# Performance work log

Measured on AMD Instinct MI355X. Metric: run time of the kernel, lower is better.

## Reference

```python
import jax, jax.numpy as jnp
import numpy as np

B, Q, V, H, U = 4, 256, 2048, 512, 128

def setup_inputs() -> dict:
    key = jax.random.key(0)
    ks = jax.random.split(key, 5)
    return {
        "queries": jax.random.normal(ks[0], (B, Q, H), dtype=jnp.float32),
        "values": jax.random.normal(ks[1], (B, V, H), dtype=jnp.float32),
        "w1": jax.random.normal(ks[2], (H, U), dtype=jnp.float32) / np.sqrt(H),
        "w2": jax.random.normal(ks[3], (H, U), dtype=jnp.float32) / np.sqrt(H),
        "v": jax.random.normal(ks[4], (U,), dtype=jnp.float32) / np.sqrt(U),
    }

def reference(queries, values, w1, w2, v):
    # Project queries and values first (cheap GEMMs), then broadcast-add.
    pq = jnp.einsum("bqh,hu->bqu", queries, w1)          # [B,Q,U]
    pv = jnp.einsum("bvh,hu->bvu", values, w2)           # [B,V,U]
    # added_qv: [B,Q,V,U] -- the large intermediate the original materializes
    scores = jnp.einsum("bqvu,u->bqv", jnp.tanh(pq[:, :, None, :] + pv[:, None, :, :]), v)
    attn = jax.nn.softmax(scores, axis=-1)               # softmax over V (last axis, as tf.nn.softmax)
    return jnp.einsum("bqv,bvh->bqh", attn, values)      # [B,Q,H]
```

## Files before the change

### kernel.cpp

```cpp
#include <hip/hip_runtime.h>

#define BB 4
#define QQ 256
#define VV 2048
#define HH 512
#define UU 128

#define C2E   2.8853900817779268f
#define LOG2E 1.4426950408889634f

__device__ __forceinline__ void fma4(float4& a, float s, const float4& w) {
    a.x = fmaf(s, w.x, a.x);
    a.y = fmaf(s, w.y, a.y);
    a.z = fmaf(s, w.z, a.z);
    a.w = fmaf(s, w.w, a.w);
}
__device__ __forceinline__ float2 rcp2(float2 x) {
    return make_float2(__builtin_amdgcn_rcpf(x.x), __builtin_amdgcn_rcpf(x.y));
}
__device__ __forceinline__ float2 mul2(float2 a, float2 b) { return make_float2(a.x*b.x, a.y*b.y); }
__device__ __forceinline__ float2 muls(float2 a, float s)  { return make_float2(a.x*s, a.y*s); }
__device__ __forceinline__ float2 fma2(float2 a, float2 b, float2 c) {
    return make_float2(fmaf(a.x, b.x, c.x), fmaf(a.y, b.y, c.y));
}
__device__ __forceinline__ float2 fmas(float2 a, float s, float2 c) {
    return make_float2(fmaf(a.x, s, c.x), fmaf(a.y, s, c.y));
}

__global__ __launch_bounds__(256) void proj_kernel(const float* __restrict__ queries,
                                                   const float* __restrict__ values,
                                                   const float* __restrict__ w1,
                                                   const float* __restrict__ w2,
                                                   float* __restrict__ pqI,
                                                   float* __restrict__ pvI,
                                                   float* __restrict__ denom) {
    __shared__ float smem[32 * 36 + 32 * 128];
    float (*As)[36] = (float(*)[36])smem;
    float* Ws = smem + 32 * 36;
    float (*Ls)[36] = (float(*)[36])smem;

    const int bid = blockIdx.x;
    const int tid = threadIdx.x;
    if (bid == 0) *(float4*)&denom[tid * 4] = make_float4(0.f, 0.f, 0.f, 0.f);

    const bool isv = (bid < 256);
    const float* A; const float* W; int b, r0, ROWS; float* Ob;
    if (isv) {
        b = bid >> 6; r0 = (bid & 63) * 32;
        A = values + ((size_t)(b * VV + r0)) * HH;  W = w2;
        Ob = pvI + (size_t)b * UU * VV;  ROWS = VV;
    } else {
        const int q = bid - 256;
        b = q >> 3; r0 = (q & 7) * 32;
        A = queries + ((size_t)(b * QQ + r0)) * HH; W = w1;
        Ob = pqI + (size_t)b * UU * QQ;  ROWS = QQ;
    }

    const int tx = tid & 31;
    const int ty = tid >> 5;
    float4 acc[4];
#pragma unroll
    for (int j = 0; j < 4; j++) acc[j] = make_float4(0.f, 0.f, 0.f, 0.f);

    for (int k0 = 0; k0 < HH; k0 += 32) {
        {
            const int r = tid >> 3, kk4 = (tid & 7) * 4;
            const float4 a = *(const float4*)&A[(size_t)r * HH + k0 + kk4];
            As[kk4 + 0][r] = a.x; As[kk4 + 1][r] = a.y;
            As[kk4 + 2][r] = a.z; As[kk4 + 3][r] = a.w;
        }
#pragma unroll
        for (int t = 0; t < 4; t++) {
            const int f = tid + t * 256;
            const int kk = f >> 5, u4 = (f & 31) * 4;
            *(float4*)&Ws[kk * 128 + u4] = *(const float4*)&W[(size_t)(k0 + kk) * UU + u4];
        }
        __syncthreads();
#pragma unroll
        for (int kk = 0; kk < 32; kk++) {
            const float4 a = *(const float4*)&As[kk][ty * 4];
            const float4 w = *(const float4*)&Ws[kk * 128 + tx * 4];
            fma4(acc[0], a.x, w);
            fma4(acc[1], a.y, w);
            fma4(acc[2], a.z, w);
            fma4(acc[3], a.w, w);
        }
        __syncthreads();
    }
#pragma unroll
    for (int j = 0; j < 4; j++) {
        const float aa[4] = {acc[j].x, acc[j].y, acc[j].z, acc[j].w};
#pragma unroll
        for (int i = 0; i < 4; i++)
            Ls[tx * 4 + i][ty * 4 + j] = __builtin_amdgcn_exp2f(aa[i] * C2E);
    }
    __syncthreads();
#pragma unroll
    for (int t = 0; t < 4; t++) {
        const int idx = tid + t * 256;
        const int g = idx >> 5, r = idx & 31;
        float4 o;
        o.x = Ls[4 * g + 0][r]; o.y = Ls[4 * g + 1][r];
        o.z = Ls[4 * g + 2][r]; o.w = Ls[4 * g + 3][r];
        *(float4*)&Ob[((size_t)g * ROWS + r0 + r) * 4] = o;
    }
}

__global__ __launch_bounds__(1024, 8) void fused_kernel(const float* __restrict__ pqI,
                                                        const float* __restrict__ pvI,
                                                        const float* __restrict__ vvec,
                                                        const float* __restrict__ values,
                                                        float* __restrict__ slab,
                                                        float* __restrict__ denom) {
    __shared__ float att[512][20];
    __shared__ float scratch[24 * 512];
    __shared__ float wred[8][16];
    const int tid = threadIdx.x;
    const int bid = blockIdx.x;
    const int vs = bid & 3, qb = (bid >> 2) & 15, b = bid >> 6;
    const int qbase = qb * 16, vbase = vs * 512;

    const int vloc = tid & 511;
    const int uh = tid >> 9;
    const int v = vbase + vloc;

    float vsum = 0.0f;
#pragma unroll
    for (int u4 = 0; u4 < UU; u4 += 4) {
        const float4 t = *(const float4*)&vvec[u4];
        vsum += t.x + t.y + t.z + t.w;
    }

    const float* pv4 = pvI + (size_t)b * UU * VV + (size_t)v * 4;
    const float* pq4 = pqI + (size_t)b * UU * QQ + (size_t)qbase * 4;

    float2 acc[8];
#pragma unroll
    for (int p = 0; p < 8; p++) acc[p] = make_float2(0.f, 0.f);

    const int G0 = uh * 16;
    float4 ev = *(const float4*)&pv4[(size_t)G0 * VV * 4];

    for (int g = 0; g < 16; g++) {
        const int G = G0 + g;
        const float* eqp = &pq4[(size_t)G * QQ * 4];
        float4 evn;
        if (g < 15) evn = *(const float4*)&pv4[(size_t)(G + 1) * VV * 4];
        const float4 wq = *(const float4*)&vvec[G * 4];
        const float w0 = 2.f * wq.x, w1 = 2.f * wq.y;
        const float w2 = 2.f * wq.z, w3 = 2.f * wq.w;
#pragma unroll
        for (int p = 0; p < 8; p++) {
            const float4 e0 = *(const float4*)&eqp[(2 * p) * 4];
            const float4 e1 = *(const float4*)&eqp[(2 * p + 1) * 4];
            const float2 a1 = make_float2(fmaf(e0.x, ev.x, 1.f), fmaf(e1.x, ev.x, 1.f));
            const float2 b1 = make_float2(fmaf(e0.y, ev.y, 1.f), fmaf(e1.y, ev.y, 1.f));
            const float2 c1 = make_float2(fmaf(e0.z, ev.z, 1.f), fmaf(e1.z, ev.z, 1.f));
            const float2 d1 = make_float2(fmaf(e0.w, ev.w, 1.f), fmaf(e1.w, ev.w, 1.f));
            const float2 pab = mul2(a1, b1), pcd = mul2(c1, d1);
            const float2 nab = fmas(a1, w1, muls(b1, w0));
            const float2 ncd = fmas(c1, w3, muls(d1, w2));
            const float2 num = fma2(nab, pcd, mul2(ncd, pab));
            const float2 den = mul2(pab, pcd);
            acc[p] = fma2(num, rcp2(den), acc[p]);
        }
        ev = evn;
    }

    float* cb = scratch;
    if (uh == 1) {
#pragma unroll
        for (int p = 0; p < 8; p++) {
            cb[(2 * p + 0) * 512 + vloc] = acc[p].x;
            cb[(2 * p + 1) * 512 + vloc] = acc[p].y;
        }
    }
    __syncthreads();
    if (uh == 0) {
#pragma unroll
        for (int p = 0; p < 8; p++) {
            const float hx = cb[(2 * p + 0) * 512 + vloc];
            const float hy = cb[(2 * p + 1) * 512 + vloc];
            float2 e;
            e.x = __builtin_amdgcn_exp2f((vsum - (acc[p].x + hx)) * LOG2E);
            e.y = __builtin_amdgcn_exp2f((vsum - (acc[p].y + hy)) * LOG2E);
            *(float2*)&att[vloc][2 * p] = e;
            acc[p] = e;
        }
#pragma unroll
        for (int off = 1; off < 64; off <<= 1) {
#pragma unroll
            for (int p = 0; p < 8; p++) {
                acc[p].x += __shfl_xor(acc[p].x, off, 64);
                acc[p].y += __shfl_xor(acc[p].y, off, 64);
            }
        }
        if ((tid & 63) == 0) {
            const int w = tid >> 6;
#pragma unroll
            for (int p = 0; p < 8; p++) {
                wred[w][2 * p + 0] = acc[p].x;
                wred[w][2 * p + 1] = acc[p].y;
            }
        }
    }
    __syncthreads();
    if (tid < 16) {
        float s = 0.f;
#pragma unroll
        for (int w = 0; w < 8; w++) s += wred[w][tid];
        atomicAdd(&denom[b * QQ + qbase + tid], s);
    }

    const int hg = tid & 127, sel = tid >> 7;
    const int qh = sel & 1, vh = sel >> 1;
    const int h0 = hg * 4;
    const float* vp = values + ((size_t)(b * VV + vbase + vh * 128)) * HH + h0;

    float4 oacc[8];
#pragma unroll
    for (int j = 0; j < 8; j++) oacc[j] = make_float4(0.f, 0.f, 0.f, 0.f);

#pragma unroll 2
    for (int vv = 0; vv < 128; vv++) {
        const float4 w = *(const float4*)&vp[(size_t)vv * HH];
        const float4 a0 = *(const float4*)&att[vh * 128 + vv][qh * 8 + 0];
        const float4 a1 = *(const float4*)&att[vh * 128 + vv][qh * 8 + 4];
        fma4(oacc[0], a0.x, w); fma4(oacc[1], a0.y, w);
        fma4(oacc[2], a0.z, w); fma4(oacc[3], a0.w, w);
        fma4(oacc[4], a1.x, w); fma4(oacc[5], a1.y, w);
        fma4(oacc[6], a1.z, w); fma4(oacc[7], a1.w, w);
    }

    float (*scr)[512] = (float(*)[512])scratch;
    for (int r = 0; r < 2; r++) {
        __syncthreads();
        if (qh == r && vh > 0) {
#pragma unroll
            for (int j = 0; j < 8; j++)
                *(float4*)&scr[(vh - 1) * 8 + j][h0] = oacc[j];
        }
        __syncthreads();
        if (qh == r && vh == 0) {
            float* sp = slab + (size_t)vs * (BB * QQ * HH);
#pragma unroll
            for (int j = 0; j < 8; j++) {
                const float4 p0 = *(const float4*)&scr[0 * 8 + j][h0];
                const float4 p1 = *(const float4*)&scr[1 * 8 + j][h0];
                const float4 p2 = *(const float4*)&scr[2 * 8 + j][h0];
                float4 o;
                o.x = oacc[j].x + p0.x + p1.x + p2.x;
                o.y = oacc[j].y + p0.y + p1.y + p2.y;
                o.z = oacc[j].z + p0.z + p1.z + p2.z;
                o.w = oacc[j].w + p0.w + p1.w + p2.w;
                *(float4*)&sp[((size_t)(b * QQ + qbase + r * 8 + j)) * HH + h0] = o;
            }
        }
    }
}

__global__ __launch_bounds__(256) void reduce_kernel(const float* __restrict__ slab,
                                                     const float* __restrict__ denom,
                                                     float* __restrict__ out) {
    const int i = blockIdx.x * 256 + threadIdx.x;
    const float r = __builtin_amdgcn_rcpf(denom[i >> 7]);
    const float4* s4 = (const float4*)slab;
    float4 s = s4[i];
#pragma unroll
    for (int k = 1; k < 4; k++) {
        const float4 p = s4[(size_t)k * (BB * QQ * HH / 4) + i];
        s.x += p.x; s.y += p.y; s.z += p.z; s.w += p.w;
    }
    s.x *= r; s.y *= r; s.z *= r; s.w *= r;
    ((float4*)out)[i] = s;
}

extern "C" void kernel_launch(void* const* d_in, const int* in_sizes, int n_in,
                              void* d_out, int out_size, void* d_ws, size_t ws_size,
                              hipStream_t stream) {
    const float* queries = (const float*)d_in[0];
    const float* values  = (const float*)d_in[1];
    const float* w1      = (const float*)d_in[2];
    const float* w2      = (const float*)d_in[3];
    const float* vvec    = (const float*)d_in[4];
    float* out = (float*)d_out;

    float* ws    = (float*)d_ws;
    float* pqI   = ws;
    float* pvI   = pqI + BB * UU * QQ;
    float* denom = pvI + (size_t)BB * UU * VV;
    float* slab  = denom + BB * QQ;

    proj_kernel<<<256 + 32, 256, 0, stream>>>(queries, values, w1, w2, pqI, pvI, denom);
    fused_kernel<<<BB * (QQ / 16) * (VV / 512), 1024, 0, stream>>>(pqI, pvI, vvec, values, slab, denom);
    reduce_kernel<<<(BB * QQ * HH) / 4 / 256, 256, 0, stream>>>(slab, denom, out);
}
```

Before: 173.8 us.

## Double-buffer proj kernel tiles with direct global-to-LDS weight loads

```diff
diff --git a/kernel.cpp b/kernel.cpp
--- a/kernel.cpp
+++ b/kernel.cpp
@@ -25,6 +25,12 @@
 }
 __device__ __forceinline__ float2 fmas(float2 a, float s, float2 c) {
     return make_float2(fmaf(a.x, s, c.x), fmaf(a.y, s, c.y));
+}
+
+typedef __attribute__((address_space(1))) const unsigned int g_u32;
+typedef __attribute__((address_space(3))) unsigned int l_u32;
+__device__ __forceinline__ void gl2lds16(const float* g, float* l) {
+    __builtin_amdgcn_global_load_lds((g_u32*)g, (l_u32*)l, 16, 0, 0);
 }
 
 __global__ __launch_bounds__(256) void proj_kernel(const float* __restrict__ queries,
@@ -34,9 +40,11 @@
                                                    float* __restrict__ pqI,
                                                    float* __restrict__ pvI,
                                                    float* __restrict__ denom) {
-    __shared__ float smem[32 * 36 + 32 * 128];
-    float (*As)[36] = (float(*)[36])smem;
-    float* Ws = smem + 32 * 36;
+    __shared__ float smem[2 * 1152 + 2 * 4096];
+    float* As0 = smem;
+    float* As1 = smem + 1152;
+    float* Ws0 = smem + 2304;
+    float* Ws1 = smem + 2304 + 4096;
     float (*Ls)[36] = (float(*)[36])smem;
 
     const int bid = blockIdx.x;
@@ -58,35 +66,59 @@
 
     const int tx = tid & 31;
     const int ty = tid >> 5;
+    const int lane = tid & 63, wv = tid >> 6;
+    const int r = tid >> 3, kk4 = (tid & 7) * 4;
+
     float4 acc[4];
 #pragma unroll
     for (int j = 0; j < 4; j++) acc[j] = make_float4(0.f, 0.f, 0.f, 0.f);
 
-    for (int k0 = 0; k0 < HH; k0 += 32) {
-        {
-            const int r = tid >> 3, kk4 = (tid & 7) * 4;
-            const float4 a = *(const float4*)&A[(size_t)r * HH + k0 + kk4];
-            As[kk4 + 0][r] = a.x; As[kk4 + 1][r] = a.y;
-            As[kk4 + 2][r] = a.z; As[kk4 + 3][r] = a.w;
-        }
-#pragma unroll
-        for (int t = 0; t < 4; t++) {
-            const int f = tid + t * 256;
-            const int kk = f >> 5, u4 = (f & 31) * 4;
-            *(float4*)&Ws[kk * 128 + u4] = *(const float4*)&W[(size_t)(k0 + kk) * UU + u4];
-        }
-        __syncthreads();
+    {
+#pragma unroll
+        for (int m = 0; m < 4; m++) {
+            const int c = wv * 4 + m;
+            gl2lds16(W + (size_t)c * 256 + lane * 4, Ws0 + c * 256);
+        }
+        const float4 a = *(const float4*)&A[(size_t)r * HH + kk4];
+        As0[(kk4 + 0) * 36 + r] = a.x; As0[(kk4 + 1) * 36 + r] = a.y;
+        As0[(kk4 + 2) * 36 + r] = a.z; As0[(kk4 + 3) * 36 + r] = a.w;
+    }
+    __syncthreads();
+
+    for (int t = 0; t < 16; t++) {
+        float* Asc = (t & 1) ? As1 : As0;
+        float* Wsc = (t & 1) ? Ws1 : Ws0;
+        float* Asn = (t & 1) ? As0 : As1;
+        float* Wsn = (t & 1) ? Ws0 : Ws1;
+
+        float4 an;
+        if (t < 15) {
+            const size_t kf = (size_t)(t + 1) * 32 * 128;
+#pragma unroll
+            for (int m = 0; m < 4; m++) {
+                const int c = wv * 4 + m;
+                gl2lds16(W + kf + (size_t)c * 256 + lane * 4, Wsn + c * 256);
+            }
+            an = *(const float4*)&A[(size_t)r * HH + (t + 1) * 32 + kk4];
+        }
+
 #pragma unroll
         for (int kk = 0; kk < 32; kk++) {
-            const float4 a = *(const float4*)&As[kk][ty * 4];
-            const float4 w = *(const float4*)&Ws[kk * 128 + tx * 4];
+            const float4 a = *(const float4*)&Asc[kk * 36 + ty * 4];
+            const float4 w = *(const float4*)&Wsc[kk * 128 + tx * 4];
             fma4(acc[0], a.x, w);
             fma4(acc[1], a.y, w);
             fma4(acc[2], a.z, w);
             fma4(acc[3], a.w, w);
         }
+
+        if (t < 15) {
+            Asn[(kk4 + 0) * 36 + r] = an.x; Asn[(kk4 + 1) * 36 + r] = an.y;
+            Asn[(kk4 + 2) * 36 + r] = an.z; Asn[(kk4 + 3) * 36 + r] = an.w;
+        }
         __syncthreads();
     }
+
 #pragma unroll
     for (int j = 0; j < 4; j++) {
         const float aa[4] = {acc[j].x, acc[j].y, acc[j].z, acc[j].w};
@@ -98,11 +130,11 @@
 #pragma unroll
     for (int t = 0; t < 4; t++) {
         const int idx = tid + t * 256;
-        const int g = idx >> 5, r = idx & 31;
+        const int g = idx >> 5, rr = idx & 31;
         float4 o;
-        o.x = Ls[4 * g + 0][r]; o.y = Ls[4 * g + 1][r];
-        o.z = Ls[4 * g + 2][r]; o.w = Ls[4 * g + 3][r];
-        *(float4*)&Ob[((size_t)g * ROWS + r0 + r) * 4] = o;
+        o.x = Ls[4 * g + 0][rr]; o.y = Ls[4 * g + 1][rr];
+        o.z = Ls[4 * g + 2][rr]; o.w = Ls[4 * g + 3][rr];
+        *(float4*)&Ob[((size_t)g * ROWS + r0 + rr) * 4] = o;
     }
 }
 
@@ -233,15 +265,15 @@
     }
 
     float (*scr)[512] = (float(*)[512])scratch;
-    for (int r = 0; r < 2; r++) {
+    for (int rr = 0; rr < 2; rr++) {
         __syncthreads();
-        if (qh == r && vh > 0) {
+        if (qh == rr && vh > 0) {
 #pragma unroll
             for (int j = 0; j < 8; j++)
                 *(float4*)&scr[(vh - 1) * 8 + j][h0] = oacc[j];
         }
         __syncthreads();
-        if (qh == r && vh == 0) {
+        if (qh == rr && vh == 0) {
             float* sp = slab + (size_t)vs * (BB * QQ * HH);
 #pragma unroll
             for (int j = 0; j < 8; j++) {
@@ -253,7 +285,7 @@
                 o.y = oacc[j].y + p0.y + p1.y + p2.y;
                 o.z = oacc[j].z + p0.z + p1.z + p2.z;
                 o.w = oacc[j].w + p0.w + p1.w + p2.w;
-                *(float4*)&sp[((size_t)(b * QQ + qbase + r * 8 + j)) * HH + h0] = o;
+                *(float4*)&sp[((size_t)(b * QQ + qbase + rr * 8 + j)) * HH + h0] = o;
             }
         }
     }
```

After: 199.7 us. 1.15x slower.
